# Kernel optimization log

Hardware: AMD Instinct MI355X
Metric: run time of the kernel (lower is better)

Reference implementation:

```python
import jax, jax.numpy as jnp
import numpy as np

N = 320      # residues (I == J)
C = 128      # c_in
H = 4        # no_heads
CH = 32      # c_hidden per head
INF = 1.0e9


def setup_inputs() -> dict:
    key = jax.random.key(0)
    ks = jax.random.split(key, 10)
    s = 0.02
    return {
        "x": jax.random.normal(ks[0], (N, N, C), dtype=jnp.float32),
        "mask": jnp.ones((N, N), dtype=jnp.float32),
        "ln_g": jnp.ones((C,), dtype=jnp.float32),
        "ln_b": jnp.zeros((C,), dtype=jnp.float32),
        "w_bias": jax.random.normal(ks[1], (C, H), dtype=jnp.float32) * s,
        "wq": jax.random.normal(ks[2], (C, H * CH), dtype=jnp.float32) * s,
        "wk": jax.random.normal(ks[3], (C, H * CH), dtype=jnp.float32) * s,
        "wv": jax.random.normal(ks[4], (C, H * CH), dtype=jnp.float32) * s,
        "wg": jax.random.normal(ks[5], (C, H * CH), dtype=jnp.float32) * s,
        "bg": jnp.ones((H * CH,), dtype=jnp.float32),  # gating bias init = 1
        "wo": jax.random.normal(ks[6], (H * CH, C), dtype=jnp.float32) * s,
        "bo": jnp.zeros((C,), dtype=jnp.float32),
    }


def _layer_norm(x, g, b, eps=1e-5):
    mu = jnp.mean(x, axis=-1, keepdims=True)
    var = jnp.var(x, axis=-1, keepdims=True)
    return (x - mu) * jax.lax.rsqrt(var + eps) * g + b


def reference(x, mask, ln_g, ln_b, w_bias, wq, wk, wv, wg, bg, wo, bo):
    # starting=True: no transpose
    x = _layer_norm(x, ln_g, ln_b)                       # [I, J, C]
    # mask bias: [I, 1, 1, J]
    mask_bias = (INF * (mask - 1.0))[:, None, None, :]
    # triangle bias: linear(x) -> [I, J, H] -> permute (2,0,1) -> [H, I, J] -> [1, H, I, J]
    tri_bias = jnp.einsum("ijc,ch->hij", x, w_bias)[None]
    # qkv projections (no bias), per-head dim CH; q scaled by 1/sqrt(CH)
    q = jnp.einsum("ijc,cd->ijd", x, wq).reshape(N, N, H, CH) / np.sqrt(CH)
    k = jnp.einsum("ijc,cd->ijd", x, wk).reshape(N, N, H, CH)
    v = jnp.einsum("ijc,cd->ijd", x, wv).reshape(N, N, H, CH)
    # scores over J (per row i): [I, H, J, J]
    scores = jnp.einsum("iqhd,ikhd->ihqk", q, k) + mask_bias + tri_bias
    a = jax.nn.softmax(scores, axis=-1)
    o = jnp.einsum("ihqk,ikhd->iqhd", a, v).reshape(N, N, H * CH)
    g = jax.nn.sigmoid(jnp.einsum("ijc,cd->ijd", x, wg) + bg)
    o = o * g
    return jnp.einsum("ijd,dc->ijc", o, wo) + bo          # [I, J, C]
```

## Files before the change

kernel.cpp:

```cpp
#include <hip/hip_runtime.h>
#include <hip/hip_bf16.h>

#define NN 320
#define CC 128
#define HH 4
#define CHD 32
#define HC 128
#define NP (NN*NN)

typedef __hip_bfloat16 bf16;
typedef __bf16 bfv8 __attribute__((ext_vector_type(8)));
typedef short bsv4 __attribute__((ext_vector_type(4)));
typedef float fv4 __attribute__((ext_vector_type(4)));

__device__ __forceinline__ unsigned short bfbits(float f) {
    bf16 h = __float2bfloat16(f);
    return *reinterpret_cast<unsigned short*>(&h);
}

__device__ __forceinline__ fv4 mfma16x16x16(bsv4 a, bsv4 b, fv4 c) {
    asm("v_mfma_f32_16x16x16_bf16 %0, %1, %2, %0" : "+v"(c) : "v"(a), "v"(b));
    return c;
}

__global__ __launch_bounds__(256) void k_wconv(
    const float* __restrict__ wq, const float* __restrict__ wk,
    const float* __restrict__ wv, const float* __restrict__ wg,
    const float* __restrict__ wo, const float* __restrict__ w_bias,
    bf16* __restrict__ wt, bf16* __restrict__ wot, bf16* __restrict__ wtb)
{
    __shared__ unsigned short T[128 * 136];
    const int b = blockIdx.x, t = threadIdx.x;
    if (b < 5) {
        const float* W = (b == 0) ? wq : (b == 1) ? wk : (b == 2) ? wv : (b == 3) ? wg : wo;
        bf16* D = (b < 4) ? (wt + b * 16384) : wot;
        const float scale = (b == 0) ? 0.17677669529663687f : 1.0f;
        for (int idx = t; idx < 16384; idx += 256) {
            int c = idx >> 7, out = idx & 127;
            T[out * 136 + c] = bfbits(W[idx] * scale);
        }
        __syncthreads();
        for (int i8 = t; i8 < 2048; i8 += 256) {
            int out = i8 >> 4, c0 = (i8 & 15) * 8;
            uint4 v = *reinterpret_cast<const uint4*>(&T[out * 136 + c0]);
            *reinterpret_cast<uint4*>(D + out * 128 + c0) = v;
        }
    } else {
        int out = t >> 4, c0 = (t & 15) * 8;
        unsigned short vals[8];
#pragma unroll
        for (int j = 0; j < 8; j++)
            vals[j] = (out < 4) ? bfbits(w_bias[(c0 + j) * 4 + out]) : (unsigned short)0;
        *reinterpret_cast<uint4*>(wtb + out * 128 + c0) = *reinterpret_cast<uint4*>(vals);
    }
}

__global__ __launch_bounds__(256) void k_proj(
    const float* __restrict__ x, const float* __restrict__ ln_g, const float* __restrict__ ln_b,
    const bf16* __restrict__ wt, const bf16* __restrict__ wtb, const float* __restrict__ bg,
    bf16* __restrict__ qo, bf16* __restrict__ ko, bf16* __restrict__ vo, bf16* __restrict__ go,
    float* __restrict__ tri)
{
    __shared__ __align__(16) unsigned short A[128 * 136];
    const int t = threadIdx.x;
    const int wv = t >> 6, lane = t & 63, g = lane >> 4, c = lane & 15;
    const size_t pb = (size_t)blockIdx.x * 128;

#pragma unroll
    for (int rnd = 0; rnd < 2; rnd++) {
        const int p = (t >> 2) + rnd * 64, l = t & 3;
        const float* xr = x + (pb + p) * CC + l * 32;
        float4 xv[8];
#pragma unroll
        for (int i = 0; i < 8; i++) xv[i] = reinterpret_cast<const float4*>(xr)[i];
        float s = 0.f, s2 = 0.f;
#pragma unroll
        for (int i = 0; i < 8; i++) {
            s  += xv[i].x + xv[i].y + xv[i].z + xv[i].w;
            s2 += xv[i].x * xv[i].x + xv[i].y * xv[i].y + xv[i].z * xv[i].z + xv[i].w * xv[i].w;
        }
        s  += __shfl_xor(s, 1, 4);  s  += __shfl_xor(s, 2, 4);
        s2 += __shfl_xor(s2, 1, 4); s2 += __shfl_xor(s2, 2, 4);
        float mu = s * (1.f / CC);
        float var = s2 * (1.f / CC) - mu * mu;
        float rstd = rsqrtf(var + 1e-5f);
        const float4* gr = reinterpret_cast<const float4*>(ln_g + l * 32);
        const float4* br = reinterpret_cast<const float4*>(ln_b + l * 32);
#pragma unroll
        for (int i = 0; i < 8; i += 2) {
            float4 g0 = gr[i], g1 = gr[i + 1], b0 = br[i], b1 = br[i + 1];
            uint4 pk;
            pk.x = (unsigned)bfbits((xv[i].x - mu) * rstd * g0.x + b0.x)
                 | ((unsigned)bfbits((xv[i].y - mu) * rstd * g0.y + b0.y) << 16);
            pk.y = (unsigned)bfbits((xv[i].z - mu) * rstd * g0.z + b0.z)
                 | ((unsigned)bfbits((xv[i].w - mu) * rstd * g0.w + b0.w) << 16);
            pk.z = (unsigned)bfbits((xv[i+1].x - mu) * rstd * g1.x + b1.x)
                 | ((unsigned)bfbits((xv[i+1].y - mu) * rstd * g1.y + b1.y) << 16);
            pk.w = (unsigned)bfbits((xv[i+1].z - mu) * rstd * g1.z + b1.z)
                 | ((unsigned)bfbits((xv[i+1].w - mu) * rstd * g1.w + b1.w) << 16);
            *reinterpret_cast<uint4*>(&A[p * 136 + l * 32 + i * 4]) = pk;
        }
    }
    __syncthreads();

    bfv8 bx[2][4];
#pragma unroll
    for (int tile = 0; tile < 2; tile++)
#pragma unroll
        for (int kc = 0; kc < 4; kc++)
            bx[tile][kc] = *reinterpret_cast<const bfv8*>(
                &A[(wv * 32 + tile * 16 + c) * 136 + kc * 32 + 8 * g]);

    fv4 zero = {0.f, 0.f, 0.f, 0.f};

    {
        fv4 at0 = zero, at1 = zero;
#pragma unroll
        for (int kc = 0; kc < 4; kc++) {
            bfv8 bb = *reinterpret_cast<const bfv8*>(wtb + c * 128 + kc * 32 + 8 * g);
            at0 = __builtin_amdgcn_mfma_f32_16x16x32_bf16(bx[0][kc], bb, at0, 0, 0, 0);
            at1 = __builtin_amdgcn_mfma_f32_16x16x32_bf16(bx[1][kc], bb, at1, 0, 0, 0);
        }
        if (c < HH) {
            float4 s0 = {at0[0], at0[1], at0[2], at0[3]};
            float4 s1 = {at1[0], at1[1], at1[2], at1[3]};
            float* tb = tri + (size_t)c * NP + pb + wv * 32 + 4 * g;
            *reinterpret_cast<float4*>(tb)      = s0;
            *reinterpret_cast<float4*>(tb + 16) = s1;
        }
    }

    __syncthreads();

    char* Wl = reinterpret_cast<char*>(A);
    bf16* Os[4] = {qo, ko, vo, go};
#pragma unroll 1
    for (int m = 0; m < 4; m++) {
        const uint4* Ws = reinterpret_cast<const uint4*>(wt + m * 16384);
#pragma unroll
        for (int j = 0; j < 8; j++) {
            int bb = t * 128 + j * 16;
            int bs = bb ^ (((bb >> 8) & 7) << 4);
            *reinterpret_cast<uint4*>(Wl + bs) = Ws[t * 8 + j];
        }
        __syncthreads();

        fv4 acc[2][8];
#pragma unroll
        for (int n = 0; n < 8; n++) { acc[0][n] = zero; acc[1][n] = zero; }
#pragma unroll
        for (int n = 0; n < 8; n++)
#pragma unroll
            for (int kc = 0; kc < 4; kc++) {
                const int row = n * 16 + c;
                const int boff = (row * 256 + kc * 64 + g * 16) ^ ((c & 7) << 4);
                bfv8 bw = *reinterpret_cast<const bfv8*>(Wl + boff);
                acc[0][n] = __builtin_amdgcn_mfma_f32_16x16x32_bf16(bw, bx[0][kc], acc[0][n], 0, 0, 0);
                acc[1][n] = __builtin_amdgcn_mfma_f32_16x16x32_bf16(bw, bx[1][kc], acc[1][n], 0, 0, 0);
            }
        if (m == 3) {
#pragma unroll
            for (int n = 0; n < 8; n++) {
                float4 bgv = *reinterpret_cast<const float4*>(bg + n * 16 + 4 * g);
                float bgs[4] = {bgv.x, bgv.y, bgv.z, bgv.w};
#pragma unroll
                for (int tile = 0; tile < 2; tile++)
#pragma unroll
                    for (int r = 0; r < 4; r++) {
                        float z = acc[tile][n][r] + bgs[r];
                        acc[tile][n][r] = 1.f / (1.f + __expf(-z));
                    }
            }
        }
        bf16* O = Os[m];
#pragma unroll
        for (int tile = 0; tile < 2; tile++)
#pragma unroll
            for (int n = 0; n < 8; n++) {
                uint2 pk;
                pk.x = (unsigned)bfbits(acc[tile][n][0]) | ((unsigned)bfbits(acc[tile][n][1]) << 16);
                pk.y = (unsigned)bfbits(acc[tile][n][2]) | ((unsigned)bfbits(acc[tile][n][3]) << 16);
                *reinterpret_cast<uint2*>(O + (pb + wv * 32 + tile * 16 + c) * HC + n * 16 + 4 * g) = pk;
            }
        __syncthreads();
    }
}

__global__ __launch_bounds__(256) void k_attn(
    const bf16* __restrict__ qi, const bf16* __restrict__ ki, const bf16* __restrict__ vi,
    const bf16* __restrict__ gi, const float* __restrict__ mask, const float* __restrict__ tri,
    bf16* __restrict__ oo)
{
    __shared__ __align__(16) unsigned VtW[32 * 164];
    __shared__ __align__(16) unsigned Kw[320 * 20];
    __shared__ __align__(16) float    Mw[320];

    const int t = threadIdx.x;
    const int w = t >> 6, lane = t & 63, g = lane >> 4, c = lane & 15;

    const int ihh = blockIdx.x;
    const int h = ihh & 3, i = ihh >> 2;
    const size_t rowbase = (size_t)i * NN;
    const float* maskrow = mask + (size_t)i * NN;

#pragma unroll
    for (int it = 0; it < 5; it++) {
        int idx = it * 256 + t;
        int key = idx >> 2, oct = idx & 3;
        uint4 kv = *reinterpret_cast<const uint4*>(ki + (rowbase + key) * HC + h * CHD + oct * 8);
        *reinterpret_cast<uint4*>(&Kw[key * 20 + oct * 4]) = kv;
    }

#pragma unroll
    for (int it = 0; it < 3; it++) {
        int idx = it * 256 + t;
        if (idx < 640) {
            int kp = idx >> 2, oct = idx & 3, d0 = oct * 8;
            const uint4 va = *reinterpret_cast<const uint4*>(vi + (rowbase + 2 * kp) * HC + h * CHD + d0);
            const uint4 vb = *reinterpret_cast<const uint4*>(vi + (rowbase + 2 * kp + 1) * HC + h * CHD + d0);
            unsigned a4[4] = {va.x, va.y, va.z, va.w};
            unsigned b4[4] = {vb.x, vb.y, vb.z, vb.w};
#pragma unroll
            for (int u2 = 0; u2 < 4; u2++) {
                int d_e = d0 + 2 * u2, d_o = d_e + 1;
                VtW[d_e * 164 + kp] = (a4[u2] & 0xffffu) | ((b4[u2] & 0xffffu) << 16);
                VtW[d_o * 164 + kp] = (a4[u2] >> 16)     | ((b4[u2] >> 16) << 16);
            }
        }
    }

    if (t < 80)
        reinterpret_cast<float4*>(Mw)[t] = reinterpret_cast<const float4*>(maskrow)[t];

    __syncthreads();

    const unsigned* Vr0 = &VtW[c * 164];
    const unsigned* Vr1 = &VtW[(16 + c) * 164];
    const unsigned* Kl  = &Kw[c * 20 + 4 * g];
    fv4 zero = {0.f, 0.f, 0.f, 0.f};

#pragma unroll 1
    for (int qt = 0; qt < 5; qt++) {
        const int qb = qt * 64 + w * 16;
        const float* trirow = tri + (size_t)h * NP + (size_t)(qb + c) * NN;
        const size_t obase  = (rowbase + qb + c) * HC + h * CHD;

        bfv8 bq = *reinterpret_cast<const bfv8*>(qi + (rowbase + qb + c) * HC + h * CHD + 8 * g);
        uint2 gg0 = *reinterpret_cast<const uint2*>(gi + obase + 4 * g);
        uint2 gg1 = *reinterpret_cast<const uint2*>(gi + obase + 16 + 4 * g);

        fv4 oa[5], ob[5];
        float mch[5], lsch[5];

        float4 trC[4];
#pragma unroll
        for (int tl = 0; tl < 4; tl++)
            trC[tl] = *reinterpret_cast<const float4*>(trirow + tl * 16 + 4 * g);

#pragma unroll
        for (int ch = 0; ch < 5; ch++) {
            const int kb = ch * 64;

            float4 trN[4];
            if (ch < 4) {
#pragma unroll
                for (int tl = 0; tl < 4; tl++)
                    trN[tl] = *reinterpret_cast<const float4*>(trirow + kb + 64 + tl * 16 + 4 * g);
            }

            bfv8 ak[4]; float4 mk[4];
#pragma unroll
            for (int tl = 0; tl < 4; tl++) {
                ak[tl] = *reinterpret_cast<const bfv8*>(Kl + (kb + tl * 16) * 20);
                mk[tl] = *reinterpret_cast<const float4*>(&Mw[kb + tl * 16 + 4 * g]);
            }

            fv4 sa[4];
#pragma unroll
            for (int tl = 0; tl < 4; tl++)
                sa[tl] = __builtin_amdgcn_mfma_f32_16x16x32_bf16(ak[tl], bq, zero, 0, 0, 0);

            float s[4][4];
#pragma unroll
            for (int tl = 0; tl < 4; tl++) {
                s[tl][0] = sa[tl][0] + trC[tl].x + fmaf(1.0e9f, mk[tl].x, -1.0e9f);
                s[tl][1] = sa[tl][1] + trC[tl].y + fmaf(1.0e9f, mk[tl].y, -1.0e9f);
                s[tl][2] = sa[tl][2] + trC[tl].z + fmaf(1.0e9f, mk[tl].z, -1.0e9f);
                s[tl][3] = sa[tl][3] + trC[tl].w + fmaf(1.0e9f, mk[tl].w, -1.0e9f);
            }

            float m01 = fmaxf(fmaxf(s[0][0], s[0][1]), fmaxf(s[0][2], s[0][3]));
            float m23 = fmaxf(fmaxf(s[1][0], s[1][1]), fmaxf(s[1][2], s[1][3]));
            float m45 = fmaxf(fmaxf(s[2][0], s[2][1]), fmaxf(s[2][2], s[2][3]));
            float m67 = fmaxf(fmaxf(s[3][0], s[3][1]), fmaxf(s[3][2], s[3][3]));
            float mt = fmaxf(fmaxf(m01, m23), fmaxf(m45, m67));
            mt = fmaxf(mt, __shfl_xor(mt, 16, 64));
            mt = fmaxf(mt, __shfl_xor(mt, 32, 64));
            mch[ch] = mt;

            float ls = 0.f;
            unsigned pw[4][2];
#pragma unroll
            for (int tl = 0; tl < 4; tl++) {
                float p0 = __expf(s[tl][0] - mt);
                float p1 = __expf(s[tl][1] - mt);
                float p2 = __expf(s[tl][2] - mt);
                float p3 = __expf(s[tl][3] - mt);
                ls += (p0 + p1) + (p2 + p3);
                pw[tl][0] = (unsigned)bfbits(p0) | ((unsigned)bfbits(p1) << 16);
                pw[tl][1] = (unsigned)bfbits(p2) | ((unsigned)bfbits(p3) << 16);
            }
            lsch[ch] = ls;

            fv4 t0 = zero, t1 = zero;
#pragma unroll
            for (int tl = 0; tl < 4; tl++) {
                union { uint2 u; bsv4 v; } a0u, a1u, pku;
                a0u.u = *reinterpret_cast<const uint2*>(Vr0 + (kb + tl * 16) / 2 + 2 * g);
                a1u.u = *reinterpret_cast<const uint2*>(Vr1 + (kb + tl * 16) / 2 + 2 * g);
                pku.u.x = pw[tl][0]; pku.u.y = pw[tl][1];
                t0 = mfma16x16x16(a0u.v, pku.v, t0);
                t1 = mfma16x16x16(a1u.v, pku.v, t1);
            }
            oa[ch] = t0; ob[ch] = t1;

            if (ch < 4) {
#pragma unroll
                for (int tl = 0; tl < 4; tl++) trC[tl] = trN[tl];
            }
        }

        float mstar = fmaxf(fmaxf(fmaxf(mch[0], mch[1]), fmaxf(mch[2], mch[3])), mch[4]);
        float e0 = __expf(mch[0] - mstar);
        float e1 = __expf(mch[1] - mstar);
        float e2 = __expf(mch[2] - mstar);
        float e3 = __expf(mch[3] - mstar);
        float e4 = __expf(mch[4] - mstar);
        float sum = lsch[0] * e0 + lsch[1] * e1 + lsch[2] * e2 + lsch[3] * e3 + lsch[4] * e4;
        sum += __shfl_xor(sum, 16, 64);
        sum += __shfl_xor(sum, 32, 64);
        float linv = 1.f / sum;

        asm volatile("s_nop 7\n\ts_nop 7"
            : "+v"(oa[0]), "+v"(oa[1]), "+v"(oa[2]), "+v"(oa[3]), "+v"(oa[4]),
              "+v"(ob[0]), "+v"(ob[1]), "+v"(ob[2]), "+v"(ob[3]), "+v"(ob[4]));

        fv4 o0, o1;
#pragma unroll
        for (int r = 0; r < 4; r++) {
            o0[r] = ((oa[0][r] * e0 + oa[1][r] * e1) + (oa[2][r] * e2 + oa[3][r] * e3)) + oa[4][r] * e4;
            o1[r] = ((ob[0][r] * e0 + ob[1][r] * e1) + (ob[2][r] * e2 + ob[3][r] * e3)) + ob[4][r] * e4;
        }

#pragma unroll
        for (int mt2 = 0; mt2 < 2; mt2++) {
            fv4 oc = mt2 ? o1 : o0;
            uint2 gg = mt2 ? gg1 : gg0;
            int d0 = mt2 * 16 + 4 * g;
            float gf0 = __uint_as_float(gg.x << 16);
            float gf1 = __uint_as_float(gg.x & 0xffff0000u);
            float gf2 = __uint_as_float(gg.y << 16);
            float gf3 = __uint_as_float(gg.y & 0xffff0000u);
            uint2 st;
            st.x = (unsigned)bfbits(oc[0] * linv * gf0) | ((unsigned)bfbits(oc[1] * linv * gf1) << 16);
            st.y = (unsigned)bfbits(oc[2] * linv * gf2) | ((unsigned)bfbits(oc[3] * linv * gf3) << 16);
            *reinterpret_cast<uint2*>(oo + obase + d0) = st;
        }
    }
}

__global__ __launch_bounds__(256) void k_out(
    const bf16* __restrict__ oi, const bf16* __restrict__ wot, const float* __restrict__ bo,
    float* __restrict__ outp)
{
    __shared__ __align__(16) char Wl[32768];
    const int t = threadIdx.x;
    const int wv = t >> 6, lane = t & 63, g = lane >> 4, c = lane & 15;
    const size_t pb = (size_t)blockIdx.x * 64;

    bfv8 bx[4];
#pragma unroll
    for (int kc = 0; kc < 4; kc++)
        bx[kc] = *reinterpret_cast<const bfv8*>(oi + (pb + wv * 16 + c) * HC + kc * 32 + 8 * g);

    const uint4* Ws = reinterpret_cast<const uint4*>(wot);
#pragma unroll
    for (int j = 0; j < 8; j++) {
        int bb = t * 128 + j * 16;
        int bs = bb ^ (((bb >> 8) & 7) << 4);
        *reinterpret_cast<uint4*>(Wl + bs) = Ws[t * 8 + j];
    }
    __syncthreads();

    fv4 zero = {0.f, 0.f, 0.f, 0.f};
    fv4 acc[8];
#pragma unroll
    for (int n = 0; n < 8; n++) acc[n] = zero;
#pragma unroll
    for (int n = 0; n < 8; n++)
#pragma unroll
        for (int kc = 0; kc < 4; kc++) {
            const int row = n * 16 + c;
            const int boff = (row * 256 + kc * 64 + g * 16) ^ ((c & 7) << 4);
            bfv8 bw = *reinterpret_cast<const bfv8*>(Wl + boff);
            acc[n] = __builtin_amdgcn_mfma_f32_16x16x32_bf16(bw, bx[kc], acc[n], 0, 0, 0);
        }
#pragma unroll
    for (int n = 0; n < 8; n++) {
        float4 b4 = *reinterpret_cast<const float4*>(bo + n * 16 + 4 * g);
        float4 st;
        st.x = acc[n][0] + b4.x;
        st.y = acc[n][1] + b4.y;
        st.z = acc[n][2] + b4.z;
        st.w = acc[n][3] + b4.w;
        *reinterpret_cast<float4*>(outp + (pb + wv * 16 + c) * CC + n * 16 + 4 * g) = st;
    }
}

extern "C" void kernel_launch(void* const* d_in, const int* in_sizes, int n_in,
                              void* d_out, int out_size, void* d_ws, size_t ws_size,
                              hipStream_t stream) {
    const float* x      = (const float*)d_in[0];
    const float* mask   = (const float*)d_in[1];
    const float* ln_g   = (const float*)d_in[2];
    const float* ln_b   = (const float*)d_in[3];
    const float* w_bias = (const float*)d_in[4];
    const float* wq     = (const float*)d_in[5];
    const float* wk     = (const float*)d_in[6];
    const float* wv     = (const float*)d_in[7];
    const float* wg     = (const float*)d_in[8];
    const float* bg     = (const float*)d_in[9];
    const float* wo     = (const float*)d_in[10];
    const float* bo     = (const float*)d_in[11];
    float* outp = (float*)d_out;

    bf16* qws = (bf16*)d_ws;
    bf16* kws = qws + (size_t)NP*HC;
    bf16* vws = kws + (size_t)NP*HC;
    bf16* gws = vws + (size_t)NP*HC;
    bf16* ows = gws + (size_t)NP*HC;
    float* tri = (float*)(ows + (size_t)NP*HC);
    bf16* wt  = (bf16*)(tri + (size_t)NP*HH);
    bf16* wot = wt + 4 * 16384;
    bf16* wtb = wot + 16384;

    hipLaunchKernelGGL(k_wconv, dim3(6), dim3(256), 0, stream,
                       wq, wk, wv, wg, wo, w_bias, wt, wot, wtb);
    hipLaunchKernelGGL(k_proj, dim3(NP/128), dim3(256), 0, stream,
                       x, ln_g, ln_b, wt, wtb, bg, qws, kws, vws, gws, tri);
    hipLaunchKernelGGL(k_attn, dim3(NN*HH), dim3(256), 0, stream,
                       qws, kws, vws, gws, mask, tri, ows);
    hipLaunchKernelGGL(k_out, dim3(NP/64), dim3(256), 0, stream,
                       ows, wot, bo, outp);
}
```

Baseline: 300.2 us.

## Split layernorm into own kernel and amortize weight staging across row tiles

LayerNorm moves out of the projection kernel into a separate kernel that writes a bf16 normalized copy of x to workspace. The projection kernel now assigns one weight matrix per block, loads it into LDS once, and loops over four 128-row tiles. The output projection likewise loops over four 64-row tiles per block. This cuts repeated weight loads and per-matrix barriers, at the cost of an extra kernel launch and a bf16 round trip of the normalized activations through global memory. Each row tile is now read from global memory by four blocks instead of once into LDS.

```diff
diff --git a/kernel.cpp b/kernel.cpp
--- a/kernel.cpp
+++ b/kernel.cpp
@@ -55,95 +55,97 @@
     }
 }
 
-__global__ __launch_bounds__(256) void k_proj(
+__global__ __launch_bounds__(256) void k_ln(
     const float* __restrict__ x, const float* __restrict__ ln_g, const float* __restrict__ ln_b,
-    const bf16* __restrict__ wt, const bf16* __restrict__ wtb, const float* __restrict__ bg,
+    bf16* __restrict__ lnb)
+{
+    const int t = threadIdx.x;
+    const int p = blockIdx.x * 64 + (t >> 2), l = t & 3;
+    const float* xr = x + (size_t)p * CC + l * 32;
+    float4 xv[8];
+#pragma unroll
+    for (int i = 0; i < 8; i++) xv[i] = reinterpret_cast<const float4*>(xr)[i];
+    float s = 0.f, s2 = 0.f;
+#pragma unroll
+    for (int i = 0; i < 8; i++) {
+        s  += xv[i].x + xv[i].y + xv[i].z + xv[i].w;
+        s2 += xv[i].x * xv[i].x + xv[i].y * xv[i].y + xv[i].z * xv[i].z + xv[i].w * xv[i].w;
+    }
+    s  += __shfl_xor(s, 1, 4);  s  += __shfl_xor(s, 2, 4);
+    s2 += __shfl_xor(s2, 1, 4); s2 += __shfl_xor(s2, 2, 4);
+    float mu = s * (1.f / CC);
+    float var = s2 * (1.f / CC) - mu * mu;
+    float rstd = rsqrtf(var + 1e-5f);
+    const float4* gr = reinterpret_cast<const float4*>(ln_g + l * 32);
+    const float4* br = reinterpret_cast<const float4*>(ln_b + l * 32);
+    bf16* dst = lnb + (size_t)p * CC + l * 32;
+#pragma unroll
+    for (int i = 0; i < 8; i += 2) {
+        float4 g0 = gr[i], g1 = gr[i + 1], b0 = br[i], b1 = br[i + 1];
+        uint4 pk;
+        pk.x = (unsigned)bfbits((xv[i].x - mu) * rstd * g0.x + b0.x)
+             | ((unsigned)bfbits((xv[i].y - mu) * rstd * g0.y + b0.y) << 16);
+        pk.y = (unsigned)bfbits((xv[i].z - mu) * rstd * g0.z + b0.z)
+             | ((unsigned)bfbits((xv[i].w - mu) * rstd * g0.w + b0.w) << 16);
+        pk.z = (unsigned)bfbits((xv[i+1].x - mu) * rstd * g1.x + b1.x)
+             | ((unsigned)bfbits((xv[i+1].y - mu) * rstd * g1.y + b1.y) << 16);
+        pk.w = (unsigned)bfbits((xv[i+1].z - mu) * rstd * g1.z + b1.z)
+             | ((unsigned)bfbits((xv[i+1].w - mu) * rstd * g1.w + b1.w) << 16);
+        *reinterpret_cast<uint4*>(dst + i * 4) = pk;
+    }
+}
+
+__global__ __launch_bounds__(256) void k_proj2(
+    const bf16* __restrict__ lnb, const bf16* __restrict__ wt, const bf16* __restrict__ wtb,
+    const float* __restrict__ bg,
     bf16* __restrict__ qo, bf16* __restrict__ ko, bf16* __restrict__ vo, bf16* __restrict__ go,
     float* __restrict__ tri)
 {
-    __shared__ __align__(16) unsigned short A[128 * 136];
+    __shared__ __align__(16) char Wl[32768];
     const int t = threadIdx.x;
     const int wv = t >> 6, lane = t & 63, g = lane >> 4, c = lane & 15;
-    const size_t pb = (size_t)blockIdx.x * 128;
-
-#pragma unroll
-    for (int rnd = 0; rnd < 2; rnd++) {
-        const int p = (t >> 2) + rnd * 64, l = t & 3;
-        const float* xr = x + (pb + p) * CC + l * 32;
-        float4 xv[8];
-#pragma unroll
-        for (int i = 0; i < 8; i++) xv[i] = reinterpret_cast<const float4*>(xr)[i];
-        float s = 0.f, s2 = 0.f;
-#pragma unroll
-        for (int i = 0; i < 8; i++) {
-            s  += xv[i].x + xv[i].y + xv[i].z + xv[i].w;
-            s2 += xv[i].x * xv[i].x + xv[i].y * xv[i].y + xv[i].z * xv[i].z + xv[i].w * xv[i].w;
-        }
-        s  += __shfl_xor(s, 1, 4);  s  += __shfl_xor(s, 2, 4);
-        s2 += __shfl_xor(s2, 1, 4); s2 += __shfl_xor(s2, 2, 4);
-        float mu = s * (1.f / CC);
-        float var = s2 * (1.f / CC) - mu * mu;
-        float rstd = rsqrtf(var + 1e-5f);
-        const float4* gr = reinterpret_cast<const float4*>(ln_g + l * 32);
-        const float4* br = reinterpret_cast<const float4*>(ln_b + l * 32);
-#pragma unroll
-        for (int i = 0; i < 8; i += 2) {
-            float4 g0 = gr[i], g1 = gr[i + 1], b0 = br[i], b1 = br[i + 1];
-            uint4 pk;
-            pk.x = (unsigned)bfbits((xv[i].x - mu) * rstd * g0.x + b0.x)
-                 | ((unsigned)bfbits((xv[i].y - mu) * rstd * g0.y + b0.y) << 16);
-            pk.y = (unsigned)bfbits((xv[i].z - mu) * rstd * g0.z + b0.z)
-                 | ((unsigned)bfbits((xv[i].w - mu) * rstd * g0.w + b0.w) << 16);
-            pk.z = (unsigned)bfbits((xv[i+1].x - mu) * rstd * g1.x + b1.x)
-                 | ((unsigned)bfbits((xv[i+1].y - mu) * rstd * g1.y + b1.y) << 16);
-            pk.w = (unsigned)bfbits((xv[i+1].z - mu) * rstd * g1.z + b1.z)
-                 | ((unsigned)bfbits((xv[i+1].w - mu) * rstd * g1.w + b1.w) << 16);
-            *reinterpret_cast<uint4*>(&A[p * 136 + l * 32 + i * 4]) = pk;
-        }
+    const int m = blockIdx.x & 3, grp = blockIdx.x >> 2;
+
+    const uint4* Ws = reinterpret_cast<const uint4*>(wt + m * 16384);
+#pragma unroll
+    for (int j = 0; j < 8; j++) {
+        int bb = t * 128 + j * 16;
+        int bs = bb ^ (((bb >> 8) & 7) << 4);
+        *reinterpret_cast<uint4*>(Wl + bs) = Ws[t * 8 + j];
     }
     __syncthreads();
 
-    bfv8 bx[2][4];
-#pragma unroll
-    for (int tile = 0; tile < 2; tile++)
-#pragma unroll
-        for (int kc = 0; kc < 4; kc++)
-            bx[tile][kc] = *reinterpret_cast<const bfv8*>(
-                &A[(wv * 32 + tile * 16 + c) * 136 + kc * 32 + 8 * g]);
-
+    bf16* O = (m == 0) ? qo : (m == 1) ? ko : (m == 2) ? vo : go;
     fv4 zero = {0.f, 0.f, 0.f, 0.f};
 
-    {
-        fv4 at0 = zero, at1 = zero;
-#pragma unroll
-        for (int kc = 0; kc < 4; kc++) {
-            bfv8 bb = *reinterpret_cast<const bfv8*>(wtb + c * 128 + kc * 32 + 8 * g);
-            at0 = __builtin_amdgcn_mfma_f32_16x16x32_bf16(bx[0][kc], bb, at0, 0, 0, 0);
-            at1 = __builtin_amdgcn_mfma_f32_16x16x32_bf16(bx[1][kc], bb, at1, 0, 0, 0);
-        }
-        if (c < HH) {
-            float4 s0 = {at0[0], at0[1], at0[2], at0[3]};
-            float4 s1 = {at1[0], at1[1], at1[2], at1[3]};
-            float* tb = tri + (size_t)c * NP + pb + wv * 32 + 4 * g;
-            *reinterpret_cast<float4*>(tb)      = s0;
-            *reinterpret_cast<float4*>(tb + 16) = s1;
-        }
-    }
-
-    __syncthreads();
-
-    char* Wl = reinterpret_cast<char*>(A);
-    bf16* Os[4] = {qo, ko, vo, go};
 #pragma unroll 1
-    for (int m = 0; m < 4; m++) {
-        const uint4* Ws = reinterpret_cast<const uint4*>(wt + m * 16384);
-#pragma unroll
-        for (int j = 0; j < 8; j++) {
-            int bb = t * 128 + j * 16;
-            int bs = bb ^ (((bb >> 8) & 7) << 4);
-            *reinterpret_cast<uint4*>(Wl + bs) = Ws[t * 8 + j];
-        }
-        __syncthreads();
+    for (int j = 0; j < 4; j++) {
+        const size_t pb = (size_t)(grp * 4 + j) * 128;
+
+        bfv8 bx[2][4];
+#pragma unroll
+        for (int tile = 0; tile < 2; tile++)
+#pragma unroll
+            for (int kc = 0; kc < 4; kc++)
+                bx[tile][kc] = *reinterpret_cast<const bfv8*>(
+                    lnb + (pb + wv * 32 + tile * 16 + c) * CC + kc * 32 + 8 * g);
+
+        if (m == 0) {
+            fv4 at0 = zero, at1 = zero;
+#pragma unroll
+            for (int kc = 0; kc < 4; kc++) {
+                bfv8 bb = *reinterpret_cast<const bfv8*>(wtb + c * 128 + kc * 32 + 8 * g);
+                at0 = __builtin_amdgcn_mfma_f32_16x16x32_bf16(bx[0][kc], bb, at0, 0, 0, 0);
+                at1 = __builtin_amdgcn_mfma_f32_16x16x32_bf16(bx[1][kc], bb, at1, 0, 0, 0);
+            }
+            if (c < HH) {
+                float4 s0 = {at0[0], at0[1], at0[2], at0[3]};
+                float4 s1 = {at1[0], at1[1], at1[2], at1[3]};
+                float* tb = tri + (size_t)c * NP + pb + wv * 32 + 4 * g;
+                *reinterpret_cast<float4*>(tb)      = s0;
+                *reinterpret_cast<float4*>(tb + 16) = s1;
+            }
+        }
 
         fv4 acc[2][8];
 #pragma unroll
@@ -172,7 +174,6 @@
                     }
             }
         }
-        bf16* O = Os[m];
 #pragma unroll
         for (int tile = 0; tile < 2; tile++)
 #pragma unroll
@@ -182,7 +183,6 @@
                 pk.y = (unsigned)bfbits(acc[tile][n][2]) | ((unsigned)bfbits(acc[tile][n][3]) << 16);
                 *reinterpret_cast<uint2*>(O + (pb + wv * 32 + tile * 16 + c) * HC + n * 16 + 4 * g) = pk;
             }
-        __syncthreads();
     }
 }
 
@@ -369,19 +369,13 @@
     }
 }
 
-__global__ __launch_bounds__(256) void k_out(
+__global__ __launch_bounds__(256) void k_out2(
     const bf16* __restrict__ oi, const bf16* __restrict__ wot, const float* __restrict__ bo,
     float* __restrict__ outp)
 {
     __shared__ __align__(16) char Wl[32768];
     const int t = threadIdx.x;
     const int wv = t >> 6, lane = t & 63, g = lane >> 4, c = lane & 15;
-    const size_t pb = (size_t)blockIdx.x * 64;
-
-    bfv8 bx[4];
-#pragma unroll
-    for (int kc = 0; kc < 4; kc++)
-        bx[kc] = *reinterpret_cast<const bfv8*>(oi + (pb + wv * 16 + c) * HC + kc * 32 + 8 * g);
 
     const uint4* Ws = reinterpret_cast<const uint4*>(wot);
 #pragma unroll
@@ -393,27 +387,38 @@
     __syncthreads();
 
     fv4 zero = {0.f, 0.f, 0.f, 0.f};
-    fv4 acc[8];
-#pragma unroll
-    for (int n = 0; n < 8; n++) acc[n] = zero;
-#pragma unroll
-    for (int n = 0; n < 8; n++)
-#pragma unroll
-        for (int kc = 0; kc < 4; kc++) {
-            const int row = n * 16 + c;
-            const int boff = (row * 256 + kc * 64 + g * 16) ^ ((c & 7) << 4);
-            bfv8 bw = *reinterpret_cast<const bfv8*>(Wl + boff);
-            acc[n] = __builtin_amdgcn_mfma_f32_16x16x32_bf16(bw, bx[kc], acc[n], 0, 0, 0);
-        }
-#pragma unroll
-    for (int n = 0; n < 8; n++) {
-        float4 b4 = *reinterpret_cast<const float4*>(bo + n * 16 + 4 * g);
-        float4 st;
-        st.x = acc[n][0] + b4.x;
-        st.y = acc[n][1] + b4.y;
-        st.z = acc[n][2] + b4.z;
-        st.w = acc[n][3] + b4.w;
-        *reinterpret_cast<float4*>(outp + (pb + wv * 16 + c) * CC + n * 16 + 4 * g) = st;
+
+#pragma unroll 1
+    for (int j = 0; j < 4; j++) {
+        const size_t pb = (size_t)(blockIdx.x * 4 + j) * 64;
+
+        bfv8 bx[4];
+#pragma unroll
+        for (int kc = 0; kc < 4; kc++)
+            bx[kc] = *reinterpret_cast<const bfv8*>(oi + (pb + wv * 16 + c) * HC + kc * 32 + 8 * g);
+
+        fv4 acc[8];
+#pragma unroll
+        for (int n = 0; n < 8; n++) acc[n] = zero;
+#pragma unroll
+        for (int n = 0; n < 8; n++)
+#pragma unroll
+            for (int kc = 0; kc < 4; kc++) {
+                const int row = n * 16 + c;
+                const int boff = (row * 256 + kc * 64 + g * 16) ^ ((c & 7) << 4);
+                bfv8 bw = *reinterpret_cast<const bfv8*>(Wl + boff);
+                acc[n] = __builtin_amdgcn_mfma_f32_16x16x32_bf16(bw, bx[kc], acc[n], 0, 0, 0);
+            }
+#pragma unroll
+        for (int n = 0; n < 8; n++) {
+            float4 b4 = *reinterpret_cast<const float4*>(bo + n * 16 + 4 * g);
+            float4 st;
+            st.x = acc[n][0] + b4.x;
+            st.y = acc[n][1] + b4.y;
+            st.z = acc[n][2] + b4.z;
+            st.w = acc[n][3] + b4.w;
+            *reinterpret_cast<float4*>(outp + (pb + wv * 16 + c) * CC + n * 16 + 4 * g) = st;
+        }
     }
 }
 
@@ -443,13 +448,16 @@
     bf16* wt  = (bf16*)(tri + (size_t)NP*HH);
     bf16* wot = wt + 4 * 16384;
     bf16* wtb = wot + 16384;
+    bf16* lnb = wtb + 2048;
 
     hipLaunchKernelGGL(k_wconv, dim3(6), dim3(256), 0, stream,
                        wq, wk, wv, wg, wo, w_bias, wt, wot, wtb);
-    hipLaunchKernelGGL(k_proj, dim3(NP/128), dim3(256), 0, stream,
-                       x, ln_g, ln_b, wt, wtb, bg, qws, kws, vws, gws, tri);
+    hipLaunchKernelGGL(k_ln, dim3(NP/64), dim3(256), 0, stream,
+                       x, ln_g, ln_b, lnb);
+    hipLaunchKernelGGL(k_proj2, dim3(800), dim3(256), 0, stream,
+                       lnb, wt, wtb, bg, qws, kws, vws, gws, tri);
     hipLaunchKernelGGL(k_attn, dim3(NN*HH), dim3(256), 0, stream,
                        qws, kws, vws, gws, mask, tri, ows);
-    hipLaunchKernelGGL(k_out, dim3(NP/64), dim3(256), 0, stream,
+    hipLaunchKernelGGL(k_out2, dim3(400), dim3(256), 0, stream,
                        ows, wot, bo, outp);
 }
```

Result: slower. 328.2 us (+9.3%).
